# Performance work log

Hardware: AMD Instinct MI355X
Metric: run time of the kernel (lower is better)

The kernel has to match this reference:

```python
import jax, jax.numpy as jnp
import numpy as np

DIM = 16  # scale_size[0] * scale_size[1]
SCALE = DIM ** -0.5


def setup_inputs() -> dict:
    key = jax.random.key(0)
    k1, k2 = jax.random.split(key)
    x = jax.random.normal(k1, (16, 256, 256, 64), dtype=jnp.float32)
    # torch Linear(dim, 2*dim, bias=False): weight shape [32, 16]
    w_qkv = jax.random.normal(k2, (32, 16), dtype=jnp.float32) * (DIM ** -0.5)
    return {"x": x, "w_qkv": w_qkv}


def reference(x, w_qkv):
    B, H, W, C = x.shape
    sh, sw = 4, 4  # scale_size
    # permute to (b, c, h, w) then adaptive avg pool to (4, 4)
    xp = jnp.transpose(x, (0, 3, 1, 2))  # [B, C, H, W]
    pooled = xp.reshape(B, C, sh, H // sh, sw, W // sw).mean(axis=(3, 5))  # [B, C, 4, 4]
    tokens = pooled.reshape(B, C, DIM)  # [B, C, 16]
    # to_qkv: Linear with weight [2*dim, dim] -> x @ W^T, then chunk
    qk = jnp.einsum('bcn,dn->bcd', tokens, w_qkv)  # [B, C, 32]
    q, k = qk[..., :DIM], qk[..., DIM:]  # each [B, C, 16]
    dots = jnp.einsum('bin,bjn->bij', q, k) * SCALE  # [B, C, C]
    attn = jax.nn.softmax(dots, axis=-1)  # [B, C, C]
    out = jnp.einsum('bhwc,btc->bhwt', x, attn)  # [B, H, W, C]
    return jax.nn.gelu(out, approximate=False)
```

## Files before the change

kernel.cpp:

```cpp
#include <hip/hip_runtime.h>
#include <math.h>
#include <cstddef>

#define BB   16
#define HH   256
#define WW   256
#define CC   64
#define NTOK 16
#define NDIM 16

#define PART_FLOATS (BB * NTOK * 16 * CC)
#define FRAG_USHORT_PER_B (8 * 64 * 8)

typedef short s16x8 __attribute__((ext_vector_type(8)));
typedef float f32x4 __attribute__((ext_vector_type(4)));

__device__ __forceinline__ unsigned short f2bf_rne(float f) {
    unsigned int u = __float_as_uint(f);
    return (unsigned short)((u + 0x7fffu + ((u >> 16) & 1u)) >> 16);
}

__global__ __launch_bounds__(256) void pool_partial(const float* __restrict__ x,
                                                    float* __restrict__ part) {
    const int blk = blockIdx.x;
    const int rc  = blk & 15;
    const int n   = (blk >> 4) & 15;
    const int b   = blk >> 8;
    const int ph  = n >> 2, pw = n & 3;
    const int t   = threadIdx.x;
    const int c4  = (t & 15) << 2;
    const int sub = t >> 4;

    const int h0 = ph * 64 + rc * 4;
    const int w0 = pw * 64;
    const float* xb = x + (((size_t)b * HH + h0) * WW + w0) * CC;

    float4 s = make_float4(0.f, 0.f, 0.f, 0.f);
#pragma unroll
    for (int k = 0; k < 16; ++k) {
        const int pos = sub + (k << 4);
        const int row = pos >> 6;
        const int col = pos & 63;
        const float4 v = *(const float4*)(xb + ((size_t)row * WW + col) * CC + c4);
        s.x += v.x; s.y += v.y; s.z += v.z; s.w += v.w;
    }

    __shared__ float lds[16 * 64];
    lds[sub * 64 + c4 + 0] = s.x;
    lds[sub * 64 + c4 + 1] = s.y;
    lds[sub * 64 + c4 + 2] = s.z;
    lds[sub * 64 + c4 + 3] = s.w;
    __syncthreads();

    if (t < 64) {
        float acc = 0.f;
#pragma unroll
        for (int ss = 0; ss < 16; ++ss) acc += lds[ss * 64 + t];
        part[(((size_t)b * NTOK + n) * 16 + rc) * CC + t] = acc;
    }
}

__global__ __launch_bounds__(256) void attn_kernel(const float* __restrict__ part,
                                                   const float* __restrict__ w_qkv,
                                                   unsigned short* __restrict__ fragw) {
    const int b = blockIdx.x;
    const int t = threadIdx.x;

    __shared__ float tok[CC * NDIM];
    __shared__ float ql [CC * NDIM];
    __shared__ float kl [CC * NDIM];
    __shared__ float dl [CC * CC];
    __shared__ float rs [CC];

    const float* pb = part + (size_t)b * NTOK * 16 * CC;

    for (int idx = t; idx < CC * NDIM; idx += 256) {
        const int c = idx >> 4, n = idx & 15;
        float a = 0.f;
#pragma unroll
        for (int rc = 0; rc < 16; ++rc) a += pb[((size_t)n * 16 + rc) * CC + c];
        tok[c * NDIM + n] = a * (1.0f / 4096.0f);
    }
    __syncthreads();

    for (int idx = t; idx < CC * 32; idx += 256) {
        const int c = idx >> 5, d = idx & 31;
        float a = 0.f;
#pragma unroll
        for (int n = 0; n < NDIM; ++n) a += tok[c * NDIM + n] * w_qkv[d * NDIM + n];
        if (d < 16) ql[c * NDIM + d] = a;
        else        kl[c * NDIM + (d - 16)] = a;
    }
    __syncthreads();

    for (int idx = t; idx < CC * CC; idx += 256) {
        const int i = idx >> 6, j = idx & 63;
        float a = 0.f;
#pragma unroll
        for (int n = 0; n < NDIM; ++n) a += ql[i * NDIM + n] * kl[j * NDIM + n];
        dl[idx] = a * 0.25f;
    }
    __syncthreads();

    if (t < CC) {
        float m = -1e30f;
        for (int j = 0; j < CC; ++j) m = fmaxf(m, dl[t * CC + j]);
        float ssum = 0.f;
        for (int j = 0; j < CC; ++j) {
            const float e = expf(dl[t * CC + j] - m);
            dl[t * CC + j] = e;
            ssum += e;
        }
        rs[t] = 1.0f / ssum;
    }
    __syncthreads();

    for (int idx = t; idx < 512; idx += 256) {
        const int tt   = idx >> 3;
        const int oct  = idx & 7;
        const int ks   = oct >> 2;
        const int g    = oct & 3;
        const int slot = (tt >> 4) * 2 + ks;
        const int lanei = (tt & 15) + g * 16;
        const float rr = rs[tt];
        s16x8 hi;
#pragma unroll
        for (int j = 0; j < 8; ++j)
            hi[j] = (short)f2bf_rne(dl[tt * CC + oct * 8 + j] * rr);
        s16x8* dst = (s16x8*)fragw + ((size_t)b * 8 + slot) * 64;
        dst[lanei] = hi;
    }
}

__device__ __forceinline__ float gelu_fast(float v) {
    const float u = v * v;
    const float z = v * fmaf(0.07135482f, u, 1.59576912f);
    const float e = exp2f(z * -1.44269504f);
    return v * __builtin_amdgcn_rcpf(e + 1.0f);
}

__device__ __forceinline__ s16x8 pack8(const float4 a, const float4 b) {
    union { unsigned int u[4]; s16x8 v; } r;
    asm("v_cvt_pk_bf16_f32 %0, %1, %2" : "=v"(r.u[0]) : "v"(a.x), "v"(a.y));
    asm("v_cvt_pk_bf16_f32 %0, %1, %2" : "=v"(r.u[1]) : "v"(a.z), "v"(a.w));
    asm("v_cvt_pk_bf16_f32 %0, %1, %2" : "=v"(r.u[2]) : "v"(b.x), "v"(b.y));
    asm("v_cvt_pk_bf16_f32 %0, %1, %2" : "=v"(r.u[3]) : "v"(b.z), "v"(b.w));
    return r.v;
}

__global__ __launch_bounds__(256) void out_mfma(const float* __restrict__ x,
                                                const unsigned short* __restrict__ frag,
                                                float* __restrict__ out) {
    const int tid  = threadIdx.x;
    const int lane = tid & 63;
    const int wv   = tid >> 6;
    const int blk  = blockIdx.x;
    const int b    = blk >> 8;
    const int row  = lane & 15;
    const int g    = lane >> 4;

    const size_t pix0 = (size_t)blk * 256 + wv * 64;
    const float* xb = x + (pix0 + row) * CC + g * 8;

    float4 a0 = *(const float4*)(xb);
    float4 a1 = *(const float4*)(xb + 4);
    float4 a2 = *(const float4*)(xb + 32);
    float4 a3 = *(const float4*)(xb + 36);

    const s16x8* fb = (const s16x8*)(frag + (size_t)b * FRAG_USHORT_PER_B);
    s16x8 bf[8];
#pragma unroll
    for (int s = 0; s < 8; ++s) bf[s] = fb[s * 64 + lane];

    const float* x1 = xb + 16 * CC;
    float4 b0 = *(const float4*)(x1);
    float4 b1 = *(const float4*)(x1 + 4);
    float4 b2 = *(const float4*)(x1 + 32);
    float4 b3 = *(const float4*)(x1 + 36);

    float* ob = out + (pix0 + (g << 2)) * CC + row;

#define TCOLS(RB, AH0, AH1)                                                     \
    _Pragma("unroll")                                                           \
    for (int tcol = 0; tcol < 4; ++tcol) {                                      \
        f32x4 acc = {0.f, 0.f, 0.f, 0.f};                                       \
        acc = __builtin_amdgcn_mfma_f32_16x16x32_bf16(AH0, bf[tcol * 2], acc, 0, 0, 0);     \
        acc = __builtin_amdgcn_mfma_f32_16x16x32_bf16(AH1, bf[tcol * 2 + 1], acc, 0, 0, 0); \
        float* o = ob + (size_t)(RB) * 16 * CC + tcol * 16;                     \
        _Pragma("unroll")                                                       \
        for (int r = 0; r < 4; ++r) o[(size_t)r * CC] = gelu_fast(acc[r]);      \
    }

    {
        const s16x8 ah0 = pack8(a0, a1);
        const s16x8 ah1 = pack8(a2, a3);
        const float* nx = xb + 32 * CC;
        a0 = *(const float4*)(nx);
        a1 = *(const float4*)(nx + 4);
        a2 = *(const float4*)(nx + 32);
        a3 = *(const float4*)(nx + 36);
        TCOLS(0, ah0, ah1)
    }
    {
        const s16x8 ah0 = pack8(b0, b1);
        const s16x8 ah1 = pack8(b2, b3);
        const float* nx = xb + 48 * CC;
        b0 = *(const float4*)(nx);
        b1 = *(const float4*)(nx + 4);
        b2 = *(const float4*)(nx + 32);
        b3 = *(const float4*)(nx + 36);
        TCOLS(1, ah0, ah1)
    }
    {
        const s16x8 ah0 = pack8(a0, a1);
        const s16x8 ah1 = pack8(a2, a3);
        TCOLS(2, ah0, ah1)
    }
    {
        const s16x8 ah0 = pack8(b0, b1);
        const s16x8 ah1 = pack8(b2, b3);
        TCOLS(3, ah0, ah1)
    }
#undef TCOLS
}

extern "C" void kernel_launch(void* const* d_in, const int* in_sizes, int n_in,
                              void* d_out, int out_size, void* d_ws, size_t ws_size,
                              hipStream_t stream) {
    const float* x     = (const float*)d_in[0];
    const float* w_qkv = (const float*)d_in[1];
    float* out   = (float*)d_out;
    float* part  = (float*)d_ws;
    unsigned short* frag = (unsigned short*)(part + PART_FLOATS);

    pool_partial<<<BB * NTOK * 16, 256, 0, stream>>>(x, part);
    attn_kernel<<<BB, 256, 0, stream>>>(part, w_qkv, frag);
    out_mfma<<<BB * 256, 256, 0, stream>>>(x, frag, out);
}
```

Before: 516.8 us.

## Split batch into two halves so x stays resident in cache between passes

Runs the pool, attention and output kernels per half-batch so the second read of x by the output kernel can hit the last-level cache instead of HBM. It also vectorises the token reduction in the attention kernel with float4 loads. The cost is twice as many kernel launches, plus serialisation gaps around the tiny attention kernel.

```diff
diff --git a/kernel.cpp b/kernel.cpp
--- a/kernel.cpp
+++ b/kernel.cpp
@@ -8,6 +8,7 @@
 #define CC   64
 #define NTOK 16
 #define NDIM 16
+#define HALF_B 8
 
 #define PART_FLOATS (BB * NTOK * 16 * CC)
 #define FRAG_USHORT_PER_B (8 * 64 * 8)
@@ -21,11 +22,12 @@
 }
 
 __global__ __launch_bounds__(256) void pool_partial(const float* __restrict__ x,
-                                                    float* __restrict__ part) {
+                                                    float* __restrict__ part,
+                                                    int b0) {
     const int blk = blockIdx.x;
     const int rc  = blk & 15;
     const int n   = (blk >> 4) & 15;
-    const int b   = blk >> 8;
+    const int b   = b0 + (blk >> 8);
     const int ph  = n >> 2, pw = n & 3;
     const int t   = threadIdx.x;
     const int c4  = (t & 15) << 2;
@@ -62,8 +64,9 @@
 
 __global__ __launch_bounds__(256) void attn_kernel(const float* __restrict__ part,
                                                    const float* __restrict__ w_qkv,
-                                                   unsigned short* __restrict__ fragw) {
-    const int b = blockIdx.x;
+                                                   unsigned short* __restrict__ fragw,
+                                                   int b0) {
+    const int b = b0 + blockIdx.x;
     const int t = threadIdx.x;
 
     __shared__ float tok[CC * NDIM];
@@ -74,12 +77,19 @@
 
     const float* pb = part + (size_t)b * NTOK * 16 * CC;
 
-    for (int idx = t; idx < CC * NDIM; idx += 256) {
-        const int c = idx >> 4, n = idx & 15;
-        float a = 0.f;
-#pragma unroll
-        for (int rc = 0; rc < 16; ++rc) a += pb[((size_t)n * 16 + rc) * CC + c];
-        tok[c * NDIM + n] = a * (1.0f / 4096.0f);
+    {
+        const int n  = t >> 4;
+        const int cq = t & 15;
+        float4 a = make_float4(0.f, 0.f, 0.f, 0.f);
+#pragma unroll
+        for (int rc = 0; rc < 16; ++rc) {
+            const float4 v = *(const float4*)(pb + ((size_t)n * 16 + rc) * CC + cq * 4);
+            a.x += v.x; a.y += v.y; a.z += v.z; a.w += v.w;
+        }
+        tok[(cq * 4 + 0) * NDIM + n] = a.x * (1.0f / 4096.0f);
+        tok[(cq * 4 + 1) * NDIM + n] = a.y * (1.0f / 4096.0f);
+        tok[(cq * 4 + 2) * NDIM + n] = a.z * (1.0f / 4096.0f);
+        tok[(cq * 4 + 3) * NDIM + n] = a.w * (1.0f / 4096.0f);
     }
     __syncthreads();
 
@@ -150,11 +160,12 @@
 
 __global__ __launch_bounds__(256) void out_mfma(const float* __restrict__ x,
                                                 const unsigned short* __restrict__ frag,
-                                                float* __restrict__ out) {
+                                                float* __restrict__ out,
+                                                int b0) {
     const int tid  = threadIdx.x;
     const int lane = tid & 63;
     const int wv   = tid >> 6;
-    const int blk  = blockIdx.x;
+    const int blk  = b0 * 256 + (int)blockIdx.x;
     const int b    = blk >> 8;
     const int row  = lane & 15;
     const int g    = lane >> 4;
@@ -173,10 +184,10 @@
     for (int s = 0; s < 8; ++s) bf[s] = fb[s * 64 + lane];
 
     const float* x1 = xb + 16 * CC;
-    float4 b0 = *(const float4*)(x1);
-    float4 b1 = *(const float4*)(x1 + 4);
-    float4 b2 = *(const float4*)(x1 + 32);
-    float4 b3 = *(const float4*)(x1 + 36);
+    float4 b0v = *(const float4*)(x1);
+    float4 b1v = *(const float4*)(x1 + 4);
+    float4 b2v = *(const float4*)(x1 + 32);
+    float4 b3v = *(const float4*)(x1 + 36);
 
     float* ob = out + (pix0 + (g << 2)) * CC + row;
 
@@ -202,13 +213,13 @@
         TCOLS(0, ah0, ah1)
     }
     {
-        const s16x8 ah0 = pack8(b0, b1);
-        const s16x8 ah1 = pack8(b2, b3);
+        const s16x8 ah0 = pack8(b0v, b1v);
+        const s16x8 ah1 = pack8(b2v, b3v);
         const float* nx = xb + 48 * CC;
-        b0 = *(const float4*)(nx);
-        b1 = *(const float4*)(nx + 4);
-        b2 = *(const float4*)(nx + 32);
-        b3 = *(const float4*)(nx + 36);
+        b0v = *(const float4*)(nx);
+        b1v = *(const float4*)(nx + 4);
+        b2v = *(const float4*)(nx + 32);
+        b3v = *(const float4*)(nx + 36);
         TCOLS(1, ah0, ah1)
     }
     {
@@ -217,8 +228,8 @@
         TCOLS(2, ah0, ah1)
     }
     {
-        const s16x8 ah0 = pack8(b0, b1);
-        const s16x8 ah1 = pack8(b2, b3);
+        const s16x8 ah0 = pack8(b0v, b1v);
+        const s16x8 ah1 = pack8(b2v, b3v);
         TCOLS(3, ah0, ah1)
     }
 #undef TCOLS
@@ -233,7 +244,10 @@
     float* part  = (float*)d_ws;
     unsigned short* frag = (unsigned short*)(part + PART_FLOATS);
 
-    pool_partial<<<BB * NTOK * 16, 256, 0, stream>>>(x, part);
-    attn_kernel<<<BB, 256, 0, stream>>>(part, w_qkv, frag);
-    out_mfma<<<BB * 256, 256, 0, stream>>>(x, frag, out);
-}
+    for (int h = 0; h < 2; ++h) {
+        const int b0 = h * HALF_B;
+        pool_partial<<<HALF_B * NTOK * 16, 256, 0, stream>>>(x, part, b0);
+        attn_kernel<<<HALF_B, 256, 0, stream>>>(part, w_qkv, frag, b0);
+        out_mfma<<<HALF_B * 256, 256, 0, stream>>>(x, frag, out, b0);
+    }
+}
```

Result: no change. 515.1 us (-0.3%).
